# Kernel tuning notes

Measured on AMD Instinct MI355X. Metric: run time of the kernel, lower is better.

Reference implementation:

```python
import jax, jax.numpy as jnp
import numpy as np

T, B, H, L, V = 256, 64, 1024, 2, 32000
Hh = H // 2
MAX_FORGET = 0.875  # forget gate z in (1-max_forget, 1)


def setup_inputs() -> dict:
    key = jax.random.key(0)
    ks = jax.random.split(key, 12)
    s = 0.02
    def w(k, shape):
        return (jax.random.normal(k, shape, jnp.float32) * s)
    return {
        "input_seq": jax.random.randint(ks[0], (T, B), 0, V),
        "h0": jax.random.normal(ks[1], (L, B, H), jnp.float32),
        "emb": w(ks[2], (V, H)),
        "W_zr1": w(ks[3], (L, H + Hh, H)),   "b_zr1": jnp.zeros((L, H), jnp.float32),
        "W_g1":  w(ks[4], (L, H + Hh, Hh)), "b_g1":  jnp.zeros((L, Hh), jnp.float32),
        "W_zr2": w(ks[5], (L, H + Hh, H)),   "b_zr2": jnp.zeros((L, H), jnp.float32),
        "W_g2":  w(ks[6], (L, H + Hh, Hh)), "b_g2":  jnp.zeros((L, Hh), jnp.float32),
    }


def _revgru_cell(x, h, Wzr1, bzr1, Wg1, bg1, Wzr2, bzr2, Wg2, bg2):
    # x: [B,H], h: [B,H] split into two halves that update each other (reversible GRU)
    h1, h2 = h[:, :Hh], h[:, Hh:]
    zr1 = jnp.concatenate([x, h2], axis=1) @ Wzr1 + bzr1
    z1 = jax.nn.sigmoid(zr1[:, :Hh]) * MAX_FORGET + (1.0 - MAX_FORGET)
    r1 = jax.nn.sigmoid(zr1[:, Hh:])
    g1 = jnp.tanh(jnp.concatenate([x, r1 * h2], axis=1) @ Wg1 + bg1)
    h1n = z1 * h1 + (1.0 - z1) * g1
    zr2 = jnp.concatenate([x, h1n], axis=1) @ Wzr2 + bzr2
    z2 = jax.nn.sigmoid(zr2[:, :Hh]) * MAX_FORGET + (1.0 - MAX_FORGET)
    r2 = jax.nn.sigmoid(zr2[:, Hh:])
    g2 = jnp.tanh(jnp.concatenate([x, r2 * h1n], axis=1) @ Wg2 + bg2)
    h2n = z2 * h2 + (1.0 - z2) * g2
    return jnp.concatenate([h1n, h2n], axis=1)


def reference(input_seq, h0, emb, W_zr1, b_zr1, W_g1, b_g1, W_zr2, b_zr2, W_g2, b_g2):
    # Dropout rates are 0 (module defaults), so all locked-dropout layers are identity.
    x_seq = emb[input_seq]  # [T,B,H]

    def step(hiddens, x_t):  # hiddens: [L,B,H]
        cur = x_t
        new = []
        for l in range(L):
            hn = _revgru_cell(cur, hiddens[l], W_zr1[l], b_zr1[l], W_g1[l], b_g1[l],
                              W_zr2[l], b_zr2[l], W_g2[l], b_g2[l])
            new.append(hn)
            cur = hn  # output_hidden feeds next layer (lockdroph is identity)
        return jnp.stack(new), None

    final, _ = jax.lax.scan(step, h0, x_seq)
    return final  # [L,B,H] last hidden per layer
```

## Files before the change

kernel.cpp:

```cpp
#include <hip/hip_runtime.h>

#define T_   256
#define B_   64
#define H_   1024
#define Hh_  512
#define L_   2
#define K1_  1536
#define MAXF 0.875f
#define NBLK 256
#define NT   1024

#define OFF_WZR1 0u
#define OFF_WG1  3145728u
#define OFF_WZR2 4718592u
#define OFF_WG2  7864320u
#define OFF_XT   9437184u
#define OFF_HT   9568256u
#define OFF_ZT   9830400u
#define OFF_RHT  9895936u
#define OFF_XC   9961472u
#define OFF_BARS 10747904u

__global__ __launch_bounds__(256) void retile_w(const float* __restrict__ src,
                                                float* __restrict__ dst,
                                                int N, int C) {
    size_t tid = (size_t)blockIdx.x * 256 + threadIdx.x;
    size_t total = (size_t)L_ * K1_ * N;
    if (tid >= total) return;
    int c = (int)(tid % C);
    int k = (int)((tid / C) % K1_);
    int b = (int)((tid / ((size_t)C * K1_)) % (N / C));
    int l = (int)(tid / ((size_t)C * K1_ * (N / C)));
    dst[tid] = src[((size_t)l * K1_ + k) * N + b * C + c];
}

__device__ __forceinline__ float ld_coh(const float* p) {
    return __hip_atomic_load(p, __ATOMIC_RELAXED, __HIP_MEMORY_SCOPE_AGENT);
}
__device__ __forceinline__ void st_coh(float* p, float v) {
    __hip_atomic_store(p, v, __ATOMIC_RELAXED, __HIP_MEMORY_SCOPE_AGENT);
}

__device__ __forceinline__ void tbar(unsigned* ctrs, int ncnt, int group,
                                     unsigned* round) {
    *round += 1;
    const unsigned need = 4u * *round;
    __syncthreads();
    if (threadIdx.x < 64) {
        if (threadIdx.x == 0)
            __hip_atomic_fetch_add(&ctrs[group], 1u, __ATOMIC_RELAXED,
                                   __HIP_MEMORY_SCOPE_AGENT);
        const int j = (int)threadIdx.x & (ncnt - 1);
        for (;;) {
            unsigned v = __hip_atomic_load(&ctrs[j], __ATOMIC_RELAXED,
                                           __HIP_MEMORY_SCOPE_AGENT);
            if (__all(v >= need)) break;
            __builtin_amdgcn_s_sleep(1);
        }
    }
    __syncthreads();
}

template<int C>
__device__ __forceinline__ float dep_gemm(const float* __restrict__ Apanel,
                                          const float* __restrict__ Wt,
                                          float* __restrict__ red) {
    const int tid  = threadIdx.x;
    const int lane = tid & 63;
    const int w    = __builtin_amdgcn_readfirstlane(tid >> 6);
    const int k0   = w * 32;
    for (int i = tid; i < 64 * (C + 1); i += NT) red[i] = 0.f;
    float av[32];
#pragma unroll
    for (int j = 0; j < 32; ++j)
        av[j] = ld_coh(Apanel + (size_t)(k0 + j) * 64 + lane);
    float acc[C];
#pragma unroll
    for (int c = 0; c < C; ++c) acc[c] = 0.f;
    __syncthreads();
#pragma unroll
    for (int j = 0; j < 32; ++j) {
        const float* wr = Wt + (size_t)(H_ + k0 + j) * C;
#pragma unroll
        for (int c = 0; c < C; ++c) acc[c] = fmaf(av[j], wr[c], acc[c]);
    }
#pragma unroll
    for (int c = 0; c < C; ++c) atomicAdd(&red[lane * (C + 1) + c], acc[c]);
    __syncthreads();
    float v = 0.f;
    if (tid < 64 * C) v = red[(tid / C) * (C + 1) + (tid % C)];
    return v;
}

__device__ __forceinline__ void helper_gemm(const float* __restrict__ Apanel,
                                            const float* __restrict__ Wz1t,
                                            const float* __restrict__ Wg1t,
                                            const float* __restrict__ Wz2t,
                                            const float* __restrict__ Wg2t,
                                            float* __restrict__ red,
                                            float* __restrict__ XcOut) {
    const int tid  = threadIdx.x;
    const int lane = tid & 63;
    const int w    = __builtin_amdgcn_readfirstlane(tid >> 6);
    const int k0   = w * 64;
    for (int i = tid; i < 64 * 49; i += NT) red[i] = 0.f;
    float acc[48];
#pragma unroll
    for (int c = 0; c < 48; ++c) acc[c] = 0.f;
    __syncthreads();
#pragma unroll 1
    for (int kb = 0; kb < 64; kb += 8) {
        float av[8];
#pragma unroll
        for (int j = 0; j < 8; ++j)
            av[j] = ld_coh(Apanel + (size_t)(k0 + kb + j) * 64 + lane);
#pragma unroll
        for (int j = 0; j < 8; ++j) {
            const int k = k0 + kb + j;
            const float* w1 = Wz1t + (size_t)k * 16;
            const float* g1 = Wg1t + (size_t)k * 8;
            const float* w2 = Wz2t + (size_t)k * 16;
            const float* g2 = Wg2t + (size_t)k * 8;
#pragma unroll
            for (int c = 0; c < 16; ++c) acc[c]      = fmaf(av[j], w1[c], acc[c]);
#pragma unroll
            for (int c = 0; c < 8;  ++c) acc[16 + c] = fmaf(av[j], g1[c], acc[16 + c]);
#pragma unroll
            for (int c = 0; c < 16; ++c) acc[24 + c] = fmaf(av[j], w2[c], acc[24 + c]);
#pragma unroll
            for (int c = 0; c < 8;  ++c) acc[40 + c] = fmaf(av[j], g2[c], acc[40 + c]);
        }
    }
#pragma unroll
    for (int c = 0; c < 48; ++c) atomicAdd(&red[lane * 49 + c], acc[c]);
    __syncthreads();
    for (int i = tid; i < 48 * 64; i += NT) {
        int cs = i >> 6, r = i & 63;
        st_coh(&XcOut[(size_t)cs * 64 + r], red[r * 49 + cs]);
    }
}

__global__ __launch_bounds__(NT) void revgru_main(
    const int* __restrict__ seq, const float* __restrict__ h0,
    const float* __restrict__ emb,
    const float* __restrict__ bzr1, const float* __restrict__ bg1,
    const float* __restrict__ bzr2, const float* __restrict__ bg2,
    float* __restrict__ ws, float* __restrict__ out)
{
    const int bi = blockIdx.x, tid = threadIdx.x;
    const bool isChain = (bi < 128);
    const int l  = isChain ? (bi >> 6) : ((bi - 128) >> 6);
    const int bl = bi & 63;
    __shared__ float red[64 * 49];
    unsigned rG = 0, rC = 0;

    float* xT  = ws + OFF_XT;
    float* hT  = ws + OFF_HT;
    float* zT  = ws + OFF_ZT;
    float* rhT = ws + OFF_RHT;
    unsigned* barC0 = (unsigned*)(ws + OFF_BARS);
    unsigned* barC1 = barC0 + 16;
    unsigned* barG  = barC0 + 32;

    const float* Wz1  = ws + OFF_WZR1 + ((size_t)l * 64 + bl) * K1_ * 16;
    const float* Wg1l = ws + OFF_WG1  + ((size_t)l * 64 + bl) * K1_ * 8;
    const float* Wz2  = ws + OFF_WZR2 + ((size_t)l * 64 + bl) * K1_ * 16;
    const float* Wg2l = ws + OFF_WG2  + ((size_t)l * 64 + bl) * K1_ * 8;

    if (bi < 128) {
        int gtid = bi * NT + tid;
        int ll = gtid >> 16, rem = gtid & 65535, r = rem >> 10, n = rem & 1023;
        st_coh(&hT[(((size_t)ll * 2 + 1) * H_ + n) * 64 + r], h0[gtid]);
    } else if (bi < 192) {
        int g2i = (bi - 128) * NT + tid;
        int k = g2i >> 6, rr = g2i & 63;
        st_coh(&xT[(size_t)k * 64 + rr], emb[(size_t)seq[rr] * H_ + k]);
    }
    tbar(barG, 64, bi >> 2, &rG);

    for (int s = 0; s <= 258; ++s) {
        if (isChain) {
            const int t = s - 1 - 2 * l;
            if (t >= 0 && t < T_) {
                const int par = t & 1;
                float* hC = hT + ((size_t)l * 2 + par) * (H_ * 64);
                float* hP = hT + ((size_t)l * 2 + (par ^ 1)) * (H_ * 64);
                float* zl  = zT  + (size_t)l * Hh_ * 64;
                float* rhl = rhT + (size_t)l * Hh_ * 64;
                const float* Xcb = ws + OFF_XC +
                    (((size_t)l * 2 + par) * 64 + bl) * (48 * 64);
                unsigned* barC = l ? barC1 : barC0;

                {
                    int r = tid >> 4, c = tid & 15, n = bl * 16 + c;
                    float xc = ld_coh(&Xcb[(size_t)c * 64 + r]) + bzr1[l * H_ + n];
                    float hv = ld_coh(&hP[(size_t)n * 64 + r]);
                    float v = dep_gemm<16>(hP + Hh_ * 64, Wz1, red) + xc;
                    float sg = 1.f / (1.f + __expf(-v));
                    if (n < Hh_) st_coh(&zl[n * 64 + r], sg * MAXF + (1.f - MAXF));
                    else st_coh(&rhl[(n - Hh_) * 64 + r], sg * hv);
                }
                tbar(barC, 16, bl >> 2, &rC);
                {
                    int tt = tid & 511, r = tt >> 3, c = tt & 7, n = bl * 8 + c;
                    float xc  = ld_coh(&Xcb[(size_t)(16 + c) * 64 + r]) + bg1[l * Hh_ + n];
                    float z   = ld_coh(&zl[n * 64 + r]);
                    float h1o = ld_coh(&hP[(size_t)n * 64 + r]);
                    float v = dep_gemm<8>(rhl, Wg1l, red);
                    if (tid < 512) {
                        float g = tanhf(v + xc);
                        st_coh(&hC[(size_t)n * 64 + r], z * h1o + (1.f - z) * g);
                    }
                }
                tbar(barC, 16, bl >> 2, &rC);
                {
                    int r = tid >> 4, c = tid & 15, n = bl * 16 + c;
                    float xc = ld_coh(&Xcb[(size_t)(24 + c) * 64 + r]) + bzr2[l * H_ + n];
                    float hv = ld_coh(&hC[(size_t)((n >= Hh_) ? (n - Hh_) : n) * 64 + r]);
                    float v = dep_gemm<16>(hC, Wz2, red) + xc;
                    float sg = 1.f / (1.f + __expf(-v));
                    if (n < Hh_) st_coh(&zl[n * 64 + r], sg * MAXF + (1.f - MAXF));
                    else st_coh(&rhl[(n - Hh_) * 64 + r], sg * hv);
                }
                tbar(barC, 16, bl >> 2, &rC);
                {
                    int tt = tid & 511, r = tt >> 3, c = tt & 7, n = bl * 8 + c;
                    float xc  = ld_coh(&Xcb[(size_t)(40 + c) * 64 + r]) + bg2[l * Hh_ + n];
                    float z   = ld_coh(&zl[n * 64 + r]);
                    float h2o = ld_coh(&hP[(size_t)(Hh_ + n) * 64 + r]);
                    float v = dep_gemm<8>(rhl, Wg2l, red);
                    if (tid < 512) {
                        float g = tanhf(v + xc);
                        st_coh(&hC[(size_t)(Hh_ + n) * 64 + r], z * h2o + (1.f - z) * g);
                    }
                }
            }
        } else {
            const int th = s - 2 * l;
            if (th >= 0 && th < T_) {
                const int par = th & 1;
                const float* Ap = (l == 0) ? (xT + (size_t)par * (H_ * 64))
                                           : (hT + (size_t)par * (H_ * 64));
                float* XcOut = ws + OFF_XC +
                    (((size_t)l * 2 + par) * 64 + bl) * (48 * 64);
                helper_gemm(Ap, Wz1, Wg1l, Wz2, Wg2l, red, XcOut);
                if (l == 0 && th + 1 < T_) {
                    int g2i = bl * NT + tid;
                    int k = g2i >> 6, rr = g2i & 63;
                    st_coh(&xT[(size_t)((th + 1) & 1) * (H_ * 64) + (size_t)k * 64 + rr],
                           emb[(size_t)seq[(th + 1) * B_ + rr] * H_ + k]);
                }
            }
        }
        tbar(barG, 64, bi >> 2, &rG);
    }
    {
        if (bi < 128) {
            int gtid = bi * NT + tid;
            int ll = gtid >> 16, rem = gtid & 65535, r = rem >> 10, n = rem & 1023;
            out[gtid] = ld_coh(&hT[(((size_t)ll * 2 + 1) * H_ + n) * 64 + r]);
        }
    }
}

extern "C" void kernel_launch(void* const* d_in, const int* in_sizes, int n_in,
                              void* d_out, int out_size, void* d_ws, size_t ws_size,
                              hipStream_t stream) {
    (void)in_sizes; (void)n_in; (void)out_size; (void)ws_size;
    const int*   seq  = (const int*)  d_in[0];
    const float* h0   = (const float*)d_in[1];
    const float* emb  = (const float*)d_in[2];
    const float* Wzr1 = (const float*)d_in[3];
    const float* bzr1 = (const float*)d_in[4];
    const float* Wg1  = (const float*)d_in[5];
    const float* bg1  = (const float*)d_in[6];
    const float* Wzr2 = (const float*)d_in[7];
    const float* bzr2 = (const float*)d_in[8];
    const float* Wg2  = (const float*)d_in[9];
    const float* bg2  = (const float*)d_in[10];
    float* out = (float*)d_out;
    float* ws  = (float*)d_ws;

    hipMemsetAsync((char*)d_ws + (size_t)OFF_BARS * 4, 0, 512, stream);
    retile_w<<<12288, 256, 0, stream>>>(Wzr1, ws + OFF_WZR1, H_, 16);
    retile_w<<<6144,  256, 0, stream>>>(Wg1,  ws + OFF_WG1,  Hh_, 8);
    retile_w<<<12288, 256, 0, stream>>>(Wzr2, ws + OFF_WZR2, H_, 16);
    retile_w<<<6144,  256, 0, stream>>>(Wg2,  ws + OFF_WG2,  Hh_, 8);

    void* args[] = { &seq, &h0, &emb, &bzr1, &bg1, &bzr2, &bg2, &ws, &out };
    hipLaunchCooperativeKernel((void*)revgru_main, dim3(NBLK), dim3(NT),
                               args, 0, stream);
}
```

Baseline: 46.99 ms.

## Shrink persistent grid to 64 blocks with wider per-block column tiles

Cuts the cooperative persistent kernel from 256 to 64 blocks. Each chain block now owns 64 (or 32) output columns and each helper block owns 192 input-projection columns, so the per-step barriers involve fewer participants. The weights are split into a recurrent part and an input-projection part, each retiled to match the new column tiles. Barrier counters are padded onto separate cache lines. The trade-off is that each block does more serial FMA work and needs more shared memory, in exchange for cheaper grid and chain synchronisation.

```diff
diff --git a/kernel.cpp b/kernel.cpp
--- a/kernel.cpp
+++ b/kernel.cpp
@@ -5,15 +5,12 @@
 #define H_   1024
 #define Hh_  512
 #define L_   2
-#define K1_  1536
 #define MAXF 0.875f
-#define NBLK 256
+#define NBLK 64
 #define NT   1024
 
-#define OFF_WZR1 0u
-#define OFF_WG1  3145728u
-#define OFF_WZR2 4718592u
-#define OFF_WG2  7864320u
+#define OFF_WX   0u
+#define OFF_WH   6291456u
 #define OFF_XT   9437184u
 #define OFF_HT   9568256u
 #define OFF_ZT   9830400u
@@ -21,17 +18,43 @@
 #define OFF_XC   9961472u
 #define OFF_BARS 10747904u
 
-__global__ __launch_bounds__(256) void retile_w(const float* __restrict__ src,
-                                                float* __restrict__ dst,
-                                                int N, int C) {
+#define WH_L  1572864u
+#define WH_P2 524288u
+#define WH_P3 786432u
+#define WH_P4 1310720u
+
+__global__ __launch_bounds__(256) void retile_wh(const float* __restrict__ src,
+                                                 float* __restrict__ dst,
+                                                 int N, int C, int Lstride) {
     size_t tid = (size_t)blockIdx.x * 256 + threadIdx.x;
-    size_t total = (size_t)L_ * K1_ * N;
+    size_t total = (size_t)L_ * 512 * N;
     if (tid >= total) return;
     int c = (int)(tid % C);
-    int k = (int)((tid / C) % K1_);
-    int b = (int)((tid / ((size_t)C * K1_)) % (N / C));
-    int l = (int)(tid / ((size_t)C * K1_ * (N / C)));
-    dst[tid] = src[((size_t)l * K1_ + k) * N + b * C + c];
+    int k = (int)((tid / C) % 512);
+    int b = (int)((tid / ((size_t)C * 512)) % 16);
+    int l = (int)(tid / ((size_t)C * 512 * 16));
+    dst[(size_t)l * Lstride + ((size_t)b * 512 + k) * C + c] =
+        src[((size_t)l * 1536 + 1024 + k) * N + b * C + c];
+}
+
+__global__ __launch_bounds__(256) void retile_wx(const float* __restrict__ Wzr1,
+                                                 const float* __restrict__ Wg1,
+                                                 const float* __restrict__ Wzr2,
+                                                 const float* __restrict__ Wg2,
+                                                 float* __restrict__ dst) {
+    size_t tid = (size_t)blockIdx.x * 256 + threadIdx.x;
+    if (tid >= (size_t)L_ * 16 * 1024 * 192) return;
+    int cm = (int)(tid % 192);
+    int k  = (int)((tid / 192) % 1024);
+    int b  = (int)((tid / (192 * 1024)) % 16);
+    int l  = (int)(tid / ((size_t)192 * 1024 * 16));
+    int cc = b * 192 + cm;
+    const float* src; int col, nc;
+    if (cc < 1024)      { src = Wzr1; col = cc;        nc = 1024; }
+    else if (cc < 1536) { src = Wg1;  col = cc - 1024; nc = 512;  }
+    else if (cc < 2560) { src = Wzr2; col = cc - 1536; nc = 1024; }
+    else                { src = Wg2;  col = cc - 2560; nc = 512;  }
+    dst[tid] = src[((size_t)l * 1536 + k) * nc + col];
 }
 
 __device__ __forceinline__ float ld_coh(const float* p) {
@@ -41,18 +64,18 @@
     __hip_atomic_store(p, v, __ATOMIC_RELAXED, __HIP_MEMORY_SCOPE_AGENT);
 }
 
-__device__ __forceinline__ void tbar(unsigned* ctrs, int ncnt, int group,
+__device__ __forceinline__ void tbar(unsigned* base, int ncnt, int group,
                                      unsigned* round) {
     *round += 1;
     const unsigned need = 4u * *round;
     __syncthreads();
     if (threadIdx.x < 64) {
         if (threadIdx.x == 0)
-            __hip_atomic_fetch_add(&ctrs[group], 1u, __ATOMIC_RELAXED,
+            __hip_atomic_fetch_add(&base[group * 16], 1u, __ATOMIC_RELAXED,
                                    __HIP_MEMORY_SCOPE_AGENT);
-        const int j = (int)threadIdx.x & (ncnt - 1);
+        const int j = ((int)threadIdx.x & (ncnt - 1)) * 16;
         for (;;) {
-            unsigned v = __hip_atomic_load(&ctrs[j], __ATOMIC_RELAXED,
+            unsigned v = __hip_atomic_load(&base[j], __ATOMIC_RELAXED,
                                            __HIP_MEMORY_SCOPE_AGENT);
             if (__all(v >= need)) break;
             __builtin_amdgcn_s_sleep(1);
@@ -62,9 +85,9 @@
 }
 
 template<int C>
-__device__ __forceinline__ float dep_gemm(const float* __restrict__ Apanel,
-                                          const float* __restrict__ Wt,
-                                          float* __restrict__ red) {
+__device__ __forceinline__ void dep_gemm(const float* __restrict__ Ap,
+                                         const float* __restrict__ Wt,
+                                         float* __restrict__ red) {
     const int tid  = threadIdx.x;
     const int lane = tid & 63;
     const int w    = __builtin_amdgcn_readfirstlane(tid >> 6);
@@ -73,70 +96,58 @@
     float av[32];
 #pragma unroll
     for (int j = 0; j < 32; ++j)
-        av[j] = ld_coh(Apanel + (size_t)(k0 + j) * 64 + lane);
+        av[j] = ld_coh(Ap + (size_t)(k0 + j) * 64 + lane);
     float acc[C];
 #pragma unroll
     for (int c = 0; c < C; ++c) acc[c] = 0.f;
     __syncthreads();
 #pragma unroll
     for (int j = 0; j < 32; ++j) {
-        const float* wr = Wt + (size_t)(H_ + k0 + j) * C;
+        const float* wr = Wt + (size_t)(k0 + j) * C;
 #pragma unroll
         for (int c = 0; c < C; ++c) acc[c] = fmaf(av[j], wr[c], acc[c]);
     }
 #pragma unroll
     for (int c = 0; c < C; ++c) atomicAdd(&red[lane * (C + 1) + c], acc[c]);
     __syncthreads();
-    float v = 0.f;
-    if (tid < 64 * C) v = red[(tid / C) * (C + 1) + (tid % C)];
-    return v;
-}
-
-__device__ __forceinline__ void helper_gemm(const float* __restrict__ Apanel,
-                                            const float* __restrict__ Wz1t,
-                                            const float* __restrict__ Wg1t,
-                                            const float* __restrict__ Wz2t,
-                                            const float* __restrict__ Wg2t,
+}
+
+__device__ __forceinline__ void helper_gemm(const float* __restrict__ Ap,
+                                            const float* __restrict__ Ws,
                                             float* __restrict__ red,
                                             float* __restrict__ XcOut) {
     const int tid  = threadIdx.x;
     const int lane = tid & 63;
     const int w    = __builtin_amdgcn_readfirstlane(tid >> 6);
-    const int k0   = w * 64;
-    for (int i = tid; i < 64 * 49; i += NT) red[i] = 0.f;
+    const int cg   = w >> 2, ks = w & 3;
+    for (int i = tid; i < 4 * 64 * 49; i += NT) red[i] = 0.f;
     float acc[48];
 #pragma unroll
     for (int c = 0; c < 48; ++c) acc[c] = 0.f;
     __syncthreads();
 #pragma unroll 1
-    for (int kb = 0; kb < 64; kb += 8) {
-        float av[8];
-#pragma unroll
-        for (int j = 0; j < 8; ++j)
-            av[j] = ld_coh(Apanel + (size_t)(k0 + kb + j) * 64 + lane);
-#pragma unroll
-        for (int j = 0; j < 8; ++j) {
-            const int k = k0 + kb + j;
-            const float* w1 = Wz1t + (size_t)k * 16;
-            const float* g1 = Wg1t + (size_t)k * 8;
-            const float* w2 = Wz2t + (size_t)k * 16;
-            const float* g2 = Wg2t + (size_t)k * 8;
-#pragma unroll
-            for (int c = 0; c < 16; ++c) acc[c]      = fmaf(av[j], w1[c], acc[c]);
-#pragma unroll
-            for (int c = 0; c < 8;  ++c) acc[16 + c] = fmaf(av[j], g1[c], acc[16 + c]);
-#pragma unroll
-            for (int c = 0; c < 16; ++c) acc[24 + c] = fmaf(av[j], w2[c], acc[24 + c]);
-#pragma unroll
-            for (int c = 0; c < 8;  ++c) acc[40 + c] = fmaf(av[j], g2[c], acc[40 + c]);
+    for (int kb = 0; kb < 256; kb += 32) {
+        float av[32];
+#pragma unroll
+        for (int j = 0; j < 32; ++j)
+            av[j] = ld_coh(Ap + (size_t)(ks * 256 + kb + j) * 64 + lane);
+#pragma unroll
+        for (int j = 0; j < 32; ++j) {
+            const float* wr = Ws + (size_t)(ks * 256 + kb + j) * 192 + cg * 48;
+#pragma unroll
+            for (int c = 0; c < 48; ++c) acc[c] = fmaf(av[j], wr[c], acc[c]);
         }
     }
 #pragma unroll
-    for (int c = 0; c < 48; ++c) atomicAdd(&red[lane * 49 + c], acc[c]);
-    __syncthreads();
-    for (int i = tid; i < 48 * 64; i += NT) {
-        int cs = i >> 6, r = i & 63;
-        st_coh(&XcOut[(size_t)cs * 64 + r], red[r * 49 + cs]);
+    for (int c = 0; c < 48; ++c)
+        atomicAdd(&red[((cg << 6) | lane) * 49 + c], acc[c]);
+    __syncthreads();
+#pragma unroll
+    for (int q = 0; q < 12; ++q) {
+        int idx = q * NT + tid;
+        int ccl = idx >> 6, r = idx & 63;
+        int cg2 = ccl / 48, c2 = ccl - cg2 * 48;
+        st_coh(&XcOut[(size_t)ccl * 64 + r], red[((cg2 << 6) | r) * 49 + c2]);
     }
 }
 
@@ -148,91 +159,108 @@
     float* __restrict__ ws, float* __restrict__ out)
 {
     const int bi = blockIdx.x, tid = threadIdx.x;
-    const bool isChain = (bi < 128);
-    const int l  = isChain ? (bi >> 6) : ((bi - 128) >> 6);
-    const int bl = bi & 63;
-    __shared__ float red[64 * 49];
+    const bool isChain = (bi < 32);
+    const int l  = (bi >> 4) & 1;
+    const int bl = bi & 15;
+    __shared__ float red[4 * 64 * 49];
     unsigned rG = 0, rC = 0;
 
     float* xT  = ws + OFF_XT;
     float* hT  = ws + OFF_HT;
     float* zT  = ws + OFF_ZT;
     float* rhT = ws + OFF_RHT;
-    unsigned* barC0 = (unsigned*)(ws + OFF_BARS);
-    unsigned* barC1 = barC0 + 16;
-    unsigned* barG  = barC0 + 32;
-
-    const float* Wz1  = ws + OFF_WZR1 + ((size_t)l * 64 + bl) * K1_ * 16;
-    const float* Wg1l = ws + OFF_WG1  + ((size_t)l * 64 + bl) * K1_ * 8;
-    const float* Wz2  = ws + OFF_WZR2 + ((size_t)l * 64 + bl) * K1_ * 16;
-    const float* Wg2l = ws + OFF_WG2  + ((size_t)l * 64 + bl) * K1_ * 8;
-
-    if (bi < 128) {
-        int gtid = bi * NT + tid;
-        int ll = gtid >> 16, rem = gtid & 65535, r = rem >> 10, n = rem & 1023;
-        st_coh(&hT[(((size_t)ll * 2 + 1) * H_ + n) * 64 + r], h0[gtid]);
-    } else if (bi < 192) {
-        int g2i = (bi - 128) * NT + tid;
-        int k = g2i >> 6, rr = g2i & 63;
-        st_coh(&xT[(size_t)k * 64 + rr], emb[(size_t)seq[rr] * H_ + k]);
-    }
-    tbar(barG, 64, bi >> 2, &rG);
+    unsigned* bars = (unsigned*)(ws + OFF_BARS);
+    unsigned* barC = bars + (l ? 64 : 0);
+    unsigned* barG = bars + 128;
+
+    const float* WhP1 = ws + OFF_WH + (size_t)l * WH_L + (size_t)bl * 512 * 64;
+    const float* WhP2 = ws + OFF_WH + (size_t)l * WH_L + WH_P2 + (size_t)bl * 512 * 32;
+    const float* WhP3 = ws + OFF_WH + (size_t)l * WH_L + WH_P3 + (size_t)bl * 512 * 64;
+    const float* WhP4 = ws + OFF_WH + (size_t)l * WH_L + WH_P4 + (size_t)bl * 512 * 32;
+    const float* Wx   = ws + OFF_WX + ((size_t)l * 16 + bl) * 1024 * 192;
+
+#pragma unroll
+    for (int q = 0; q < 2; ++q) {
+        int g = bi * 2048 + q * NT + tid;
+        int ll = g >> 16, rem = g & 65535, r = rem >> 10, n = rem & 1023;
+        st_coh(&hT[(((size_t)ll * 2 + 1) * H_ + n) * 64 + r], h0[g]);
+    }
+    {
+        int gx = bi * NT + tid;
+        int k = gx >> 6, rr = gx & 63;
+        st_coh(&xT[gx], emb[(size_t)seq[rr] * H_ + k]);
+    }
+    tbar(barG, 16, bi >> 2, &rG);
 
     for (int s = 0; s <= 258; ++s) {
         if (isChain) {
             const int t = s - 1 - 2 * l;
-            if (t >= 0 && t < T_) {
-                const int par = t & 1;
-                float* hC = hT + ((size_t)l * 2 + par) * (H_ * 64);
-                float* hP = hT + ((size_t)l * 2 + (par ^ 1)) * (H_ * 64);
-                float* zl  = zT  + (size_t)l * Hh_ * 64;
-                float* rhl = rhT + (size_t)l * Hh_ * 64;
-                const float* Xcb = ws + OFF_XC +
-                    (((size_t)l * 2 + par) * 64 + bl) * (48 * 64);
-                unsigned* barC = l ? barC1 : barC0;
-
-                {
-                    int r = tid >> 4, c = tid & 15, n = bl * 16 + c;
-                    float xc = ld_coh(&Xcb[(size_t)c * 64 + r]) + bzr1[l * H_ + n];
-                    float hv = ld_coh(&hP[(size_t)n * 64 + r]);
-                    float v = dep_gemm<16>(hP + Hh_ * 64, Wz1, red) + xc;
+            const bool act = (t >= 0) && (t < T_);
+            const int par = t & 1;
+            float* hC = hT + ((size_t)l * 2 + (t & 1)) * (H_ * 64);
+            float* hP = hT + ((size_t)l * 2 + ((t & 1) ^ 1)) * (H_ * 64);
+            float* zl  = zT  + (size_t)l * Hh_ * 64;
+            float* rhl = rhT + (size_t)l * Hh_ * 64;
+            const float* Xcb = ws + OFF_XC + ((size_t)l * 2 + par) * (3072 * 64);
+
+            if (act) {
+                dep_gemm<64>(hP + Hh_ * 64, WhP1, red);
+#pragma unroll
+                for (int q = 0; q < 4; ++q) {
+                    int idx = q * NT + tid;
+                    int c = idx >> 6, r = idx & 63, n = bl * 64 + c;
+                    float v = red[r * 65 + c] + ld_coh(&Xcb[(size_t)n * 64 + r])
+                            + bzr1[l * H_ + n];
                     float sg = 1.f / (1.f + __expf(-v));
-                    if (n < Hh_) st_coh(&zl[n * 64 + r], sg * MAXF + (1.f - MAXF));
-                    else st_coh(&rhl[(n - Hh_) * 64 + r], sg * hv);
-                }
-                tbar(barC, 16, bl >> 2, &rC);
-                {
-                    int tt = tid & 511, r = tt >> 3, c = tt & 7, n = bl * 8 + c;
-                    float xc  = ld_coh(&Xcb[(size_t)(16 + c) * 64 + r]) + bg1[l * Hh_ + n];
-                    float z   = ld_coh(&zl[n * 64 + r]);
+                    if (n < Hh_) st_coh(&zl[(size_t)n * 64 + r], sg * MAXF + (1.f - MAXF));
+                    else st_coh(&rhl[(size_t)(n - Hh_) * 64 + r],
+                                sg * ld_coh(&hP[(size_t)n * 64 + r]));
+                }
+            }
+            tbar(barC, 4, bl >> 2, &rC);
+            if (act) {
+                dep_gemm<32>(rhl, WhP2, red);
+#pragma unroll
+                for (int q = 0; q < 2; ++q) {
+                    int idx = q * NT + tid;
+                    int c = idx >> 6, r = idx & 63, n = bl * 32 + c;
+                    float g = tanhf(red[r * 33 + c]
+                                    + ld_coh(&Xcb[(size_t)(1024 + n) * 64 + r])
+                                    + bg1[l * Hh_ + n]);
+                    float z   = ld_coh(&zl[(size_t)n * 64 + r]);
                     float h1o = ld_coh(&hP[(size_t)n * 64 + r]);
-                    float v = dep_gemm<8>(rhl, Wg1l, red);
-                    if (tid < 512) {
-                        float g = tanhf(v + xc);
-                        st_coh(&hC[(size_t)n * 64 + r], z * h1o + (1.f - z) * g);
-                    }
-                }
-                tbar(barC, 16, bl >> 2, &rC);
-                {
-                    int r = tid >> 4, c = tid & 15, n = bl * 16 + c;
-                    float xc = ld_coh(&Xcb[(size_t)(24 + c) * 64 + r]) + bzr2[l * H_ + n];
-                    float hv = ld_coh(&hC[(size_t)((n >= Hh_) ? (n - Hh_) : n) * 64 + r]);
-                    float v = dep_gemm<16>(hC, Wz2, red) + xc;
+                    st_coh(&hC[(size_t)n * 64 + r], z * h1o + (1.f - z) * g);
+                }
+            }
+            tbar(barC, 4, bl >> 2, &rC);
+            if (act) {
+                dep_gemm<64>(hC, WhP3, red);
+#pragma unroll
+                for (int q = 0; q < 4; ++q) {
+                    int idx = q * NT + tid;
+                    int c = idx >> 6, r = idx & 63, n = bl * 64 + c;
+                    float v = red[r * 65 + c]
+                            + ld_coh(&Xcb[(size_t)(1536 + n) * 64 + r])
+                            + bzr2[l * H_ + n];
                     float sg = 1.f / (1.f + __expf(-v));
-                    if (n < Hh_) st_coh(&zl[n * 64 + r], sg * MAXF + (1.f - MAXF));
-                    else st_coh(&rhl[(n - Hh_) * 64 + r], sg * hv);
-                }
-                tbar(barC, 16, bl >> 2, &rC);
-                {
-                    int tt = tid & 511, r = tt >> 3, c = tt & 7, n = bl * 8 + c;
-                    float xc  = ld_coh(&Xcb[(size_t)(40 + c) * 64 + r]) + bg2[l * Hh_ + n];
-                    float z   = ld_coh(&zl[n * 64 + r]);
+                    if (n < Hh_) st_coh(&zl[(size_t)n * 64 + r], sg * MAXF + (1.f - MAXF));
+                    else st_coh(&rhl[(size_t)(n - Hh_) * 64 + r],
+                                sg * ld_coh(&hC[(size_t)(n - Hh_) * 64 + r]));
+                }
+            }
+            tbar(barC, 4, bl >> 2, &rC);
+            if (act) {
+                dep_gemm<32>(rhl, WhP4, red);
+#pragma unroll
+                for (int q = 0; q < 2; ++q) {
+                    int idx = q * NT + tid;
+                    int c = idx >> 6, r = idx & 63, n = bl * 32 + c;
+                    float g = tanhf(red[r * 33 + c]
+                                    + ld_coh(&Xcb[(size_t)(2560 + n) * 64 + r])
+                                    + bg2[l * Hh_ + n]);
+                    float z   = ld_coh(&zl[(size_t)n * 64 + r]);
                     float h2o = ld_coh(&hP[(size_t)(Hh_ + n) * 64 + r]);
-                    float v = dep_gemm<8>(rhl, Wg2l, red);
-                    if (tid < 512) {
-                        float g = tanhf(v + xc);
-                        st_coh(&hC[(size_t)(Hh_ + n) * 64 + r], z * h2o + (1.f - z) * g);
-                    }
+                    st_coh(&hC[(size_t)(Hh_ + n) * 64 + r], z * h2o + (1.f - z) * g);
                 }
             }
         } else {
@@ -242,24 +270,26 @@
                 const float* Ap = (l == 0) ? (xT + (size_t)par * (H_ * 64))
                                            : (hT + (size_t)par * (H_ * 64));
                 float* XcOut = ws + OFF_XC +
-                    (((size_t)l * 2 + par) * 64 + bl) * (48 * 64);
-                helper_gemm(Ap, Wz1, Wg1l, Wz2, Wg2l, red, XcOut);
+                    (((size_t)l * 2 + par) * 3072 + (size_t)bl * 192) * 64;
+                helper_gemm(Ap, Wx, red, XcOut);
                 if (l == 0 && th + 1 < T_) {
-                    int g2i = bl * NT + tid;
-                    int k = g2i >> 6, rr = g2i & 63;
-                    st_coh(&xT[(size_t)((th + 1) & 1) * (H_ * 64) + (size_t)k * 64 + rr],
-                           emb[(size_t)seq[(th + 1) * B_ + rr] * H_ + k]);
+#pragma unroll
+                    for (int q = 0; q < 4; ++q) {
+                        int idx = bl * 4096 + q * NT + tid;
+                        int k = idx >> 6, rr = idx & 63;
+                        st_coh(&xT[(size_t)((th + 1) & 1) * (H_ * 64) + idx],
+                               emb[(size_t)seq[(th + 1) * B_ + rr] * H_ + k]);
+                    }
                 }
             }
         }
-        tbar(barG, 64, bi >> 2, &rG);
-    }
-    {
-        if (bi < 128) {
-            int gtid = bi * NT + tid;
-            int ll = gtid >> 16, rem = gtid & 65535, r = rem >> 10, n = rem & 1023;
-            out[gtid] = ld_coh(&hT[(((size_t)ll * 2 + 1) * H_ + n) * 64 + r]);
-        }
+        tbar(barG, 16, bi >> 2, &rG);
+    }
+#pragma unroll
+    for (int q = 0; q < 2; ++q) {
+        int g = bi * 2048 + q * NT + tid;
+        int ll = g >> 16, rem = g & 65535, r = rem >> 10, n = rem & 1023;
+        out[g] = ld_coh(&hT[(((size_t)ll * 2 + 1) * H_ + n) * 64 + r]);
     }
 }
 
@@ -281,11 +311,12 @@
     float* out = (float*)d_out;
     float* ws  = (float*)d_ws;
 
-    hipMemsetAsync((char*)d_ws + (size_t)OFF_BARS * 4, 0, 512, stream);
-    retile_w<<<12288, 256, 0, stream>>>(Wzr1, ws + OFF_WZR1, H_, 16);
-    retile_w<<<6144,  256, 0, stream>>>(Wg1,  ws + OFF_WG1,  Hh_, 8);
-    retile_w<<<12288, 256, 0, stream>>>(Wzr2, ws + OFF_WZR2, H_, 16);
-    retile_w<<<6144,  256, 0, stream>>>(Wg2,  ws + OFF_WG2,  Hh_, 8);
+    hipMemsetAsync((char*)d_ws + (size_t)OFF_BARS * 4, 0, 2048, stream);
+    retile_wx<<<24576, 256, 0, stream>>>(Wzr1, Wg1, Wzr2, Wg2, ws + OFF_WX);
+    retile_wh<<<4096, 256, 0, stream>>>(Wzr1, ws + OFF_WH, 1024, 64, WH_L);
+    retile_wh<<<2048, 256, 0, stream>>>(Wg1,  ws + OFF_WH + WH_P2, 512, 32, WH_L);
+    retile_wh<<<4096, 256, 0, stream>>>(Wzr2, ws + OFF_WH + WH_P3, 1024, 64, WH_L);
+    retile_wh<<<2048, 256, 0, stream>>>(Wg2,  ws + OFF_WH + WH_P4, 512, 32, WH_L);
 
     void* args[] = { &seq, &h0, &emb, &bzr1, &bg1, &bzr2, &bg2, &ws, &out };
     hipLaunchCooperativeKernel((void*)revgru_main, dim3(NBLK), dim3(NT),
```

Measured after the change: 121.1 ms. 158% more time.
